# Performance work log

Hardware: AMD Instinct MI355X
Metric: run time of the kernel (lower is better)

The kernel has to match this reference:

```python
import jax, jax.numpy as jnp
import numpy as np

N_NODES = 100000
N_EDGES = 1600000
D_FEAT = 128
HIDDEN = 256
N_CLASSES = 40


def setup_inputs() -> dict:
    key = jax.random.key(0)
    ks = jax.random.split(key, 6)
    x = jax.random.normal(ks[0], (N_NODES, D_FEAT), dtype=jnp.float32)
    edge_index = jax.random.randint(ks[1], (2, N_EDGES), 0, N_NODES, dtype=jnp.int32)
    # Glorot-ish scaled weights
    w1_l = jax.random.normal(ks[2], (HIDDEN, D_FEAT), dtype=jnp.float32) / np.sqrt(D_FEAT)
    w1_r = jax.random.normal(ks[3], (HIDDEN, D_FEAT), dtype=jnp.float32) / np.sqrt(D_FEAT)
    w2_l = jax.random.normal(ks[4], (N_CLASSES, HIDDEN), dtype=jnp.float32) / np.sqrt(HIDDEN)
    w2_r = jax.random.normal(ks[5], (N_CLASSES, HIDDEN), dtype=jnp.float32) / np.sqrt(HIDDEN)
    b1_l = jnp.zeros((HIDDEN,), jnp.float32)
    b2_l = jnp.zeros((N_CLASSES,), jnp.float32)
    return {"x": x, "edge_index": edge_index, "w1_l": w1_l, "b1_l": b1_l,
            "w1_r": w1_r, "w2_l": w2_l, "b2_l": b2_l, "w2_r": w2_r}


def _sage_conv(x, src, dst, n_nodes, w_l, b_l, w_r):
    # mean aggregation of source-node features onto target nodes
    msg = x[src]                                                  # [E, d]
    agg = jax.ops.segment_sum(msg, dst, num_segments=n_nodes)     # [N, d]
    cnt = jax.ops.segment_sum(jnp.ones((dst.shape[0], 1), x.dtype), dst,
                              num_segments=n_nodes)               # [N, 1]
    agg = agg / jnp.maximum(cnt, 1.0)
    # out = lin_l(agg) + lin_r(x); lin_l has bias, lin_r does not (PyG default)
    return agg @ w_l.T + b_l + x @ w_r.T


def reference(x, edge_index, w1_l, b1_l, w1_r, w2_l, b2_l, w2_r):
    n_nodes = x.shape[0]
    src, dst = edge_index[0], edge_index[1]
    h = jax.nn.relu(_sage_conv(x, src, dst, n_nodes, w1_l, b1_l, w1_r))
    # dropout is identity in eval mode
    out = _sage_conv(h, src, dst, n_nodes, w2_l, b2_l, w2_r)
    return jax.nn.log_softmax(out, axis=1)
```

## Files before the change

kernel.cpp:

```cpp
#include <hip/hip_runtime.h>
#include <hip/hip_bf16.h>
#include <stdint.h>

#define NN 100000
#define NE 1600000
#define DF 128
#define DH 256
#define NC 40
#define BSHIFT 8
#define NBKT 391
#define EPB 8192
#define NBIN_BLOCKS ((NE + EPB - 1) / EPB)

typedef __attribute__((ext_vector_type(8))) short short8;
typedef __attribute__((ext_vector_type(4))) float f32x4;

typedef const __attribute__((address_space(1))) unsigned int* gas1;
typedef __attribute__((address_space(3))) unsigned int* las3;

__device__ __forceinline__ void gload16(const void* g, void* l) {
  __builtin_amdgcn_global_load_lds((gas1)g, (las3)l, 16, 0, 0);
}

__device__ __forceinline__ unsigned short f2bf(float f) {
  union { float f; unsigned u; } v; v.f = f;
  unsigned r = v.u + 0x7FFFu + ((v.u >> 16) & 1u);
  return (unsigned short)(r >> 16);
}
__device__ __forceinline__ float bflo(unsigned u) {
  union { unsigned u; float f; } v; v.u = u << 16; return v.f;
}
__device__ __forceinline__ float bfhi(unsigned u) {
  union { unsigned u; float f; } v; v.u = u & 0xFFFF0000u; return v.f;
}

__global__ void k_xbf16(const float* __restrict__ x, unsigned* __restrict__ xb) {
  int i = blockIdx.x * blockDim.x + threadIdx.x;
  if (i < NN * 64) {
    float2 v = ((const float2*)x)[i];
    xb[i] = ((unsigned)f2bf(v.y) << 16) | f2bf(v.x);
  }
}

__global__ __launch_bounds__(256) void k_bhist(const int* __restrict__ dst, int* __restrict__ bcnt) {
  __shared__ int h[NBKT];
  int tid = threadIdx.x;
  for (int b = tid; b < NBKT; b += 256) h[b] = 0;
  __syncthreads();
  int base = blockIdx.x * EPB;
  int n = NE - base; if (n > EPB) n = EPB;
  for (int i = tid; i < n; i += 256) atomicAdd(&h[dst[base + i] >> BSHIFT], 1);
  __syncthreads();
  for (int b = tid; b < NBKT; b += 256) if (h[b]) atomicAdd(&bcnt[b], h[b]);
}

__global__ __launch_bounds__(512) void k_bscan(const int* __restrict__ bcnt,
                                               int* __restrict__ boff, int* __restrict__ bcur) {
  __shared__ int s[512];
  int tid = threadIdx.x;
  int v = (tid < NBKT) ? bcnt[tid] : 0;
  s[tid] = v;
  __syncthreads();
  for (int off = 1; off < 512; off <<= 1) {
    int a = (tid >= off) ? s[tid - off] : 0;
    __syncthreads();
    s[tid] += a;
    __syncthreads();
  }
  int excl = s[tid] - v;
  if (tid < NBKT) { boff[tid] = excl; bcur[tid] = excl; }
  if (tid == 0) boff[NBKT] = s[511];
}

__global__ __launch_bounds__(256) void k_bin(const int* __restrict__ src, const int* __restrict__ dst,
                                             int* __restrict__ bcur, unsigned* __restrict__ pairs) {
  __shared__ int hcnt[NBKT];
  __shared__ int hbase[NBKT];
  int tid = threadIdx.x;
  for (int b = tid; b < NBKT; b += 256) hcnt[b] = 0;
  __syncthreads();
  int base = blockIdx.x * EPB;
  int n = NE - base; if (n > EPB) n = EPB;
  for (int i = tid; i < n; i += 256) atomicAdd(&hcnt[dst[base + i] >> BSHIFT], 1);
  __syncthreads();
  for (int b = tid; b < NBKT; b += 256) hbase[b] = hcnt[b] ? atomicAdd(&bcur[b], hcnt[b]) : 0;
  __syncthreads();
  for (int b = tid; b < NBKT; b += 256) hcnt[b] = 0;
  __syncthreads();
  for (int i = tid; i < n; i += 256) {
    int s = src[base + i], d = dst[base + i];
    int b = d >> BSHIFT;
    int slot = atomicAdd(&hcnt[b], 1);
    pairs[hbase[b] + slot] = (unsigned)s | ((unsigned)(d & 255) << 17);
  }
}

__global__ __launch_bounds__(256) void k_csr(const unsigned* __restrict__ pairs,
                                             const int* __restrict__ boff,
                                             int* __restrict__ row_ptr, int* __restrict__ csr) {
  __shared__ int ncnt[256];
  __shared__ int noff[256];
  int tid = threadIdx.x;
  int b = blockIdx.x;
  int base = boff[b], end = boff[b + 1];
  ncnt[tid] = 0;
  __syncthreads();
  for (int e = base + tid; e < end; e += 256) atomicAdd(&ncnt[pairs[e] >> 17], 1);
  __syncthreads();
  int v = ncnt[tid];
  noff[tid] = v;
  __syncthreads();
  for (int off = 1; off < 256; off <<= 1) {
    int a = (tid >= off) ? noff[tid - off] : 0;
    __syncthreads();
    noff[tid] += a;
    __syncthreads();
  }
  int excl = noff[tid] - v;
  __syncthreads();
  noff[tid] = excl;
  ncnt[tid] = 0;
  __syncthreads();
  int gnode = (b << BSHIFT) + tid;
  if (gnode < NN) row_ptr[gnode] = base + excl;
  if (b == NBKT - 1 && tid == 0) row_ptr[NN] = NE;
  for (int e = base + tid; e < end; e += 256) {
    unsigned p = pairs[e];
    int ld = p >> 17;
    int slot = atomicAdd(&ncnt[ld], 1);
    csr[base + noff[ld] + slot] = (int)(p & 0x1FFFFu);
  }
}

__global__ void k_packw(const float* __restrict__ w1l, const float* __restrict__ w1r,
                        const float* __restrict__ w2l, const float* __restrict__ w2r,
                        unsigned short* __restrict__ Wc, unsigned short* __restrict__ W2c) {
  int i = blockIdx.x * blockDim.x + threadIdx.x;
  if (i < 256 * 256) {
    int o = i >> 8, k = i & 255;
    float v = (k < 128) ? w1l[o * 128 + k] : w1r[o * 128 + (k - 128)];
    Wc[i] = f2bf(v);
  }
  int j = i - 256 * 256;
  if (j >= 0 && j < 80 * 256) {
    int o = j >> 8, k = j & 255;
    float v = (o < 40) ? w2l[o * 256 + k] : w2r[(o - 40) * 256 + k];
    W2c[j] = f2bf(v);
  }
}

__global__ void k_agg1(const unsigned* __restrict__ xb, const int* __restrict__ row_ptr,
                       const int* __restrict__ csr_src, unsigned* __restrict__ A1) {
  int w = threadIdx.x >> 6, lane = threadIdx.x & 63;
  int node = blockIdx.x * 4 + w;
  if (node >= NN) return;
  int rs = row_ptr[node], re = row_ptr[node + 1];
  float a0 = 0.f, a1 = 0.f;
  for (int e = rs; e < re; e += 8) {
    unsigned v[8];
#pragma unroll
    for (int j = 0; j < 8; ++j) {
      int ej = e + j;
      int idx = csr_src[ej < re ? ej : re - 1];
      unsigned t = xb[(size_t)idx * 64 + lane];
      v[j] = (ej < re) ? t : 0u;
    }
#pragma unroll
    for (int j = 0; j < 8; ++j) { a0 += bflo(v[j]); a1 += bfhi(v[j]); }
  }
  int deg = re - rs;
  float inv = 1.f / (float)(deg > 0 ? deg : 1);
  unsigned pack = ((unsigned)f2bf(a1 * inv) << 16) | f2bf(a0 * inv);
  A1[(size_t)node * 64 + lane] = pack;
}

__global__ __launch_bounds__(256) void k_fused(const unsigned short* __restrict__ A1,
                                               const unsigned short* __restrict__ XB,
                                               const unsigned short* __restrict__ Wc,
                                               const float* __restrict__ b1,
                                               const unsigned short* __restrict__ W2c,
                                               unsigned short* __restrict__ Pb,
                                               float* __restrict__ R) {
  __shared__ __align__(16) unsigned short sA[64 * 64];
  __shared__ __align__(16) unsigned short sB[256 * 64];
  __shared__ __align__(16) unsigned short sH[64 * 256];
  int tid = threadIdx.x;
  int w = tid >> 6, lane = tid & 63;
  int brow = blockIdx.x * 64;
  int wr = (w >> 1) * 32, wc = (w & 1) * 128;
  f32x4 acc[2][8] = {};

  for (int kt = 0; kt < 4; ++kt) {
    const unsigned short* srcA = (kt < 2) ? A1 : XB;
    int kcol = (kt & 1) * 64;
#pragma unroll
    for (int t = 0; t < 2; ++t) {
      int c = t * 256 + tid;
      int r = c >> 3, cc = c & 7;
      int scc = cc ^ (r & 7);
      int gr = brow + r; if (gr > NN - 1) gr = NN - 1;
      gload16(srcA + (size_t)gr * 128 + kcol + scc * 8, sA + c * 8);
    }
#pragma unroll
    for (int t = 0; t < 8; ++t) {
      int c = t * 256 + tid;
      int r = c >> 3, cc = c & 7;
      int scc = cc ^ (r & 7);
      gload16(Wc + (size_t)r * 256 + kt * 64 + scc * 8, sB + c * 8);
    }
    __syncthreads();
#pragma unroll
    for (int kg = 0; kg < 2; ++kg) {
      short8 af[2], bfr[8];
#pragma unroll
      for (int m = 0; m < 2; ++m) {
        int row = wr + m * 16 + (lane & 15);
        int cch = (kg * 4 + (lane >> 4)) ^ (row & 7);
        af[m] = *(const short8*)(sA + row * 64 + cch * 8);
      }
#pragma unroll
      for (int n = 0; n < 8; ++n) {
        int row = wc + n * 16 + (lane & 15);
        int cch = (kg * 4 + (lane >> 4)) ^ (row & 7);
        bfr[n] = *(const short8*)(sB + row * 64 + cch * 8);
      }
#pragma unroll
      for (int m = 0; m < 2; ++m)
#pragma unroll
        for (int n = 0; n < 8; ++n)
          acc[m][n] = __builtin_amdgcn_mfma_f32_16x16x32_bf16(af[m], bfr[n], acc[m][n], 0, 0, 0);
    }
    __syncthreads();
  }

  {
    int colbase = wc + (lane & 15);
    int rowb = wr + (lane >> 4) * 4;
#pragma unroll
    for (int n = 0; n < 8; ++n) {
      int col = colbase + n * 16;
      float bias = b1[col];
      int g = col >> 3, off = col & 7;
#pragma unroll
      for (int m = 0; m < 2; ++m) {
        int row0 = rowb + m * 16;
#pragma unroll
        for (int q = 0; q < 4; ++q) {
          int row = row0 + q;
          float v = acc[m][n][q] + bias;
          v = v > 0.f ? v : 0.f;
          sH[row * 256 + ((g ^ (row & 7)) << 3) + off] = f2bf(v);
        }
      }
    }
  }
  __syncthreads();

  f32x4 a2[5] = {};
  int nrow = w * 16 + (lane & 15);
  for (int kt = 0; kt < 4; ++kt) {
#pragma unroll
    for (int t = 0; t < 3; ++t) {
      int c = t * 256 + tid;
      if (c < 640) {
        int r = c >> 3, cc = c & 7;
        int scc = cc ^ (r & 7);
        gload16(W2c + (size_t)r * 256 + kt * 64 + scc * 8, sB + c * 8);
      }
    }
    __syncthreads();
#pragma unroll
    for (int kg = 0; kg < 2; ++kg) {
      int gH = kt * 8 + kg * 4 + (lane >> 4);
      short8 bf1 = *(const short8*)(sH + nrow * 256 + ((gH ^ (nrow & 7)) << 3));
      short8 af[5];
#pragma unroll
      for (int m = 0; m < 5; ++m) {
        int arow = m * 16 + (lane & 15);
        int cch = (kg * 4 + (lane >> 4)) ^ (arow & 7);
        af[m] = *(const short8*)(sB + arow * 64 + cch * 8);
      }
#pragma unroll
      for (int m = 0; m < 5; ++m)
        a2[m] = __builtin_amdgcn_mfma_f32_16x16x32_bf16(af[m], bf1, a2[m], 0, 0, 0);
    }
    __syncthreads();
  }

  int node = brow + nrow;
  if (node < NN) {
#pragma unroll
    for (int m = 0; m < 5; ++m) {
      int c0 = m * 16 + (lane >> 4) * 4;
      f32x4 v = a2[m];
      if (c0 < NC) {
        uint2 pk;
        pk.x = ((unsigned)f2bf(v[1]) << 16) | f2bf(v[0]);
        pk.y = ((unsigned)f2bf(v[3]) << 16) | f2bf(v[2]);
        *(uint2*)(Pb + (size_t)node * 64 + c0) = pk;
      } else {
        if (c0 < 64) *(uint2*)(Pb + (size_t)node * 64 + c0) = make_uint2(0u, 0u);
        *(float4*)(R + (size_t)node * NC + (c0 - NC)) = make_float4(v[0], v[1], v[2], v[3]);
      }
    }
  }
}

__global__ __launch_bounds__(256) void k_final(const unsigned short* __restrict__ Pb,
                                               const float* __restrict__ R,
                                               const int* __restrict__ row_ptr,
                                               const int* __restrict__ csr_src,
                                               const float* __restrict__ b2,
                                               float* __restrict__ out) {
  int w = threadIdx.x >> 6, lane = threadIdx.x & 63;
  int g = lane >> 4, r = lane & 15;
  int node = blockIdx.x * 4 + w;
  if (node >= NN) return;
  int rs = row_ptr[node], re = row_ptr[node + 1];
  float s0 = 0.f, s1 = 0.f, s2 = 0.f, s3 = 0.f;
  int nfull = (re - rs) >> 3;
  int e = rs + g;
  for (int it = 0; it < nfull; ++it, e += 8) {
    int sa = csr_src[e];
    int sb = csr_src[e + 4];
    uint2 va = *(const uint2*)(Pb + (size_t)sa * 64 + r * 4);
    uint2 vb = *(const uint2*)(Pb + (size_t)sb * 64 + r * 4);
    s0 += bflo(va.x) + bflo(vb.x);
    s1 += bfhi(va.x) + bfhi(vb.x);
    s2 += bflo(va.y) + bflo(vb.y);
    s3 += bfhi(va.y) + bfhi(vb.y);
  }
  if (e < re) {
    int sa = csr_src[e];
    uint2 va = *(const uint2*)(Pb + (size_t)sa * 64 + r * 4);
    s0 += bflo(va.x); s1 += bfhi(va.x); s2 += bflo(va.y); s3 += bfhi(va.y);
  }
  e += 4;
  if (e < re) {
    int sa = csr_src[e];
    uint2 va = *(const uint2*)(Pb + (size_t)sa * 64 + r * 4);
    s0 += bflo(va.x); s1 += bfhi(va.x); s2 += bflo(va.y); s3 += bfhi(va.y);
  }
  s0 += __shfl_xor(s0, 16); s0 += __shfl_xor(s0, 32);
  s1 += __shfl_xor(s1, 16); s1 += __shfl_xor(s1, 32);
  s2 += __shfl_xor(s2, 16); s2 += __shfl_xor(s2, 32);
  s3 += __shfl_xor(s3, 16); s3 += __shfl_xor(s3, 32);

  int deg = re - rs;
  float inv = 1.f / (float)(deg > 0 ? deg : 1);
  bool act = r < 10;
  float4 rr = act ? *(const float4*)(R + (size_t)node * NC + r * 4) : make_float4(0, 0, 0, 0);
  float4 bb = act ? *(const float4*)(b2 + r * 4) : make_float4(0, 0, 0, 0);
  float v0 = s0 * inv + rr.x + bb.x;
  float v1 = s1 * inv + rr.y + bb.y;
  float v2 = s2 * inv + rr.z + bb.z;
  float v3 = s3 * inv + rr.w + bb.w;
  float mx = act ? fmaxf(fmaxf(v0, v1), fmaxf(v2, v3)) : -1e30f;
#pragma unroll
  for (int o = 1; o < 16; o <<= 1) mx = fmaxf(mx, __shfl_xor(mx, o));
  float ex = act ? (__expf(v0 - mx) + __expf(v1 - mx) + __expf(v2 - mx) + __expf(v3 - mx)) : 0.f;
#pragma unroll
  for (int o = 1; o < 16; o <<= 1) ex += __shfl_xor(ex, o);
  float ls = mx + __logf(ex);
  if (g == 0 && act) {
    float4 o4 = make_float4(v0 - ls, v1 - ls, v2 - ls, v3 - ls);
    *(float4*)(out + (size_t)node * NC + r * 4) = o4;
  }
}

extern "C" void kernel_launch(void* const* d_in, const int* in_sizes, int n_in,
                              void* d_out, int out_size, void* d_ws, size_t ws_size,
                              hipStream_t stream) {
  const float* x   = (const float*)d_in[0];
  const int*   ei  = (const int*)d_in[1];
  const float* w1l = (const float*)d_in[2];
  const float* b1  = (const float*)d_in[3];
  const float* w1r = (const float*)d_in[4];
  const float* w2l = (const float*)d_in[5];
  const float* b2  = (const float*)d_in[6];
  const float* w2r = (const float*)d_in[7];
  float* out = (float*)d_out;
  const int* src = ei;
  const int* dst = ei + NE;

  char* ws = (char*)d_ws;
  size_t off = 0;
  auto alloc = [&](size_t bytes) -> char* {
    char* p = ws + off;
    off = (off + bytes + 255) & ~(size_t)255;
    return p;
  };
  int* bcnt     = (int*)alloc((size_t)(NBKT + 1) * 4);
  int* boff     = (int*)alloc((size_t)(NBKT + 1) * 4);
  int* bcur     = (int*)alloc((size_t)NBKT * 4);
  int* row_ptr  = (int*)alloc((size_t)(NN + 1) * 4);
  unsigned* pairs = (unsigned*)alloc((size_t)NE * 4);
  int* csr      = (int*)alloc((size_t)NE * 4);
  unsigned short* Wc  = (unsigned short*)alloc(256 * 256 * 2);
  unsigned short* W2c = (unsigned short*)alloc(80 * 256 * 2);
  unsigned*       xb  = (unsigned*)alloc((size_t)NN * 64 * 4);
  unsigned*       A1  = (unsigned*)alloc((size_t)NN * 64 * 4);
  unsigned short* Pb  = (unsigned short*)alloc((size_t)NN * 64 * 2);
  float*          R   = (float*)alloc((size_t)NN * NC * 4);

  hipMemsetAsync(bcnt, 0, (size_t)(NBKT + 1) * 4, stream);
  k_bhist<<<NBIN_BLOCKS, 256, 0, stream>>>(dst, bcnt);
  k_xbf16<<<(NN * 64 + 255) / 256, 256, 0, stream>>>(x, xb);
  k_bscan<<<1, 512, 0, stream>>>(bcnt, boff, bcur);
  k_bin<<<NBIN_BLOCKS, 256, 0, stream>>>(src, dst, bcur, pairs);
  k_csr<<<NBKT, 256, 0, stream>>>(pairs, boff, row_ptr, csr);
  k_packw<<<336, 256, 0, stream>>>(w1l, w1r, w2l, w2r, Wc, W2c);
  k_agg1<<<(NN + 3) / 4, 256, 0, stream>>>(xb, row_ptr, csr, A1);
  k_fused<<<(NN + 63) / 64, 256, 0, stream>>>((const unsigned short*)A1,
                                              (const unsigned short*)xb, Wc, b1, W2c, Pb, R);
  k_final<<<(NN + 3) / 4, 256, 0, stream>>>(Pb, R, row_ptr, csr, b2, out);
}
```

Before: 323.4 us.

## Pad CSR rows to multiples of eight with dummy zero node

Rebuilds the CSR so each node's neighbor list is padded to a multiple of 8 entries, filled with an index to an extra all-zero row appended to the bf16 feature and Pb buffers. Degrees are stored separately. The aggregation kernels can then drop their tail handling and bounds checks. k_agg1 now has each half-wave read a different edge with 8-byte loads and combines the halves with a shuffle. The cost is extra padded gathers (up to 7 per node), which always hit the same cached zero row, plus a larger CSR buffer with fixed per-bucket slack that assumes no bucket needs more than 2048 padding slots.

```diff
diff --git a/kernel.cpp b/kernel.cpp
--- a/kernel.cpp
+++ b/kernel.cpp
@@ -11,6 +11,7 @@
 #define NBKT 391
 #define EPB 8192
 #define NBIN_BLOCKS ((NE + EPB - 1) / EPB)
+#define BKT_SLACK 2048
 
 typedef __attribute__((ext_vector_type(8))) short short8;
 typedef __attribute__((ext_vector_type(4))) float f32x4;
@@ -36,9 +37,13 @@
 
 __global__ void k_xbf16(const float* __restrict__ x, unsigned* __restrict__ xb) {
   int i = blockIdx.x * blockDim.x + threadIdx.x;
-  if (i < NN * 64) {
-    float2 v = ((const float2*)x)[i];
-    xb[i] = ((unsigned)f2bf(v.y) << 16) | f2bf(v.x);
+  if (i < (NN + 1) * 64) {
+    unsigned pk = 0u;
+    if (i < NN * 64) {
+      float2 v = ((const float2*)x)[i];
+      pk = ((unsigned)f2bf(v.y) << 16) | f2bf(v.x);
+    }
+    xb[i] = pk;
   }
 }
 
@@ -55,7 +60,8 @@
 }
 
 __global__ __launch_bounds__(512) void k_bscan(const int* __restrict__ bcnt,
-                                               int* __restrict__ boff, int* __restrict__ bcur) {
+                                               int* __restrict__ boff, int* __restrict__ bcur,
+                                               unsigned short* __restrict__ Pb) {
   __shared__ int s[512];
   int tid = threadIdx.x;
   int v = (tid < NBKT) ? bcnt[tid] : 0;
@@ -69,7 +75,8 @@
   }
   int excl = s[tid] - v;
   if (tid < NBKT) { boff[tid] = excl; bcur[tid] = excl; }
-  if (tid == 0) boff[NBKT] = s[511];
+  if (tid == NBKT) boff[NBKT] = excl;
+  if (tid >= 448 && tid < 480) ((unsigned*)(Pb + (size_t)NN * 64))[tid - 448] = 0u;
 }
 
 __global__ __launch_bounds__(256) void k_bin(const int* __restrict__ src, const int* __restrict__ dst,
@@ -97,18 +104,21 @@
 
 __global__ __launch_bounds__(256) void k_csr(const unsigned* __restrict__ pairs,
                                              const int* __restrict__ boff,
-                                             int* __restrict__ row_ptr, int* __restrict__ csr) {
+                                             int* __restrict__ deg, int* __restrict__ row_ptr8,
+                                             int* __restrict__ csr8) {
   __shared__ int ncnt[256];
   __shared__ int noff[256];
   int tid = threadIdx.x;
   int b = blockIdx.x;
   int base = boff[b], end = boff[b + 1];
+  int base8 = base + BKT_SLACK * b;
   ncnt[tid] = 0;
   __syncthreads();
   for (int e = base + tid; e < end; e += 256) atomicAdd(&ncnt[pairs[e] >> 17], 1);
   __syncthreads();
-  int v = ncnt[tid];
-  noff[tid] = v;
+  int cnt = ncnt[tid];
+  int pcnt = (cnt + 7) & ~7;
+  noff[tid] = pcnt;
   __syncthreads();
   for (int off = 1; off < 256; off <<= 1) {
     int a = (tid >= off) ? noff[tid - off] : 0;
@@ -116,20 +126,20 @@
     noff[tid] += a;
     __syncthreads();
   }
-  int excl = noff[tid] - v;
-  __syncthreads();
-  noff[tid] = excl;
+  int pexcl = noff[tid] - pcnt;
+  __syncthreads();
+  noff[tid] = pexcl;
   ncnt[tid] = 0;
   __syncthreads();
   int gnode = (b << BSHIFT) + tid;
-  if (gnode < NN) row_ptr[gnode] = base + excl;
-  if (b == NBKT - 1 && tid == 0) row_ptr[NN] = NE;
+  if (gnode < NN) { deg[gnode] = cnt; row_ptr8[gnode] = base8 + pexcl; }
   for (int e = base + tid; e < end; e += 256) {
     unsigned p = pairs[e];
     int ld = p >> 17;
     int slot = atomicAdd(&ncnt[ld], 1);
-    csr[base + noff[ld] + slot] = (int)(p & 0x1FFFFu);
-  }
+    csr8[base8 + noff[ld] + slot] = (int)(p & 0x1FFFFu);
+  }
+  for (int k = cnt; k < pcnt; ++k) csr8[base8 + pexcl + k] = NN;
 }
 
 __global__ void k_packw(const float* __restrict__ w1l, const float* __restrict__ w1r,
@@ -149,29 +159,38 @@
   }
 }
 
-__global__ void k_agg1(const unsigned* __restrict__ xb, const int* __restrict__ row_ptr,
-                       const int* __restrict__ csr_src, unsigned* __restrict__ A1) {
+__global__ void k_agg1(const unsigned* __restrict__ xb, const int* __restrict__ row_ptr8,
+                       const int* __restrict__ deg, const int* __restrict__ csr8,
+                       unsigned* __restrict__ A1) {
   int w = threadIdx.x >> 6, lane = threadIdx.x & 63;
   int node = blockIdx.x * 4 + w;
   if (node >= NN) return;
-  int rs = row_ptr[node], re = row_ptr[node + 1];
-  float a0 = 0.f, a1 = 0.f;
-  for (int e = rs; e < re; e += 8) {
-    unsigned v[8];
-#pragma unroll
-    for (int j = 0; j < 8; ++j) {
-      int ej = e + j;
-      int idx = csr_src[ej < re ? ej : re - 1];
-      unsigned t = xb[(size_t)idx * 64 + lane];
-      v[j] = (ej < re) ? t : 0u;
-    }
-#pragma unroll
-    for (int j = 0; j < 8; ++j) { a0 += bflo(v[j]); a1 += bfhi(v[j]); }
-  }
-  int deg = re - rs;
-  float inv = 1.f / (float)(deg > 0 ? deg : 1);
-  unsigned pack = ((unsigned)f2bf(a1 * inv) << 16) | f2bf(a0 * inv);
-  A1[(size_t)node * 64 + lane] = pack;
+  int dg = deg[node];
+  int rs = row_ptr8[node];
+  int pdeg = (dg + 7) & ~7;
+  int half = lane >> 5, li = lane & 31;
+  float a0 = 0.f, a1 = 0.f, a2 = 0.f, a3 = 0.f;
+  const unsigned* xp = xb + li * 2;
+  for (int e = rs; e < rs + pdeg; e += 8) {
+#pragma unroll
+    for (int j = 0; j < 4; ++j) {
+      int idx = csr8[e + 2 * j + half];
+      uint2 v = *(const uint2*)(xp + (size_t)idx * 64);
+      a0 += bflo(v.x); a1 += bfhi(v.x);
+      a2 += bflo(v.y); a3 += bfhi(v.y);
+    }
+  }
+  a0 += __shfl_xor(a0, 32);
+  a1 += __shfl_xor(a1, 32);
+  a2 += __shfl_xor(a2, 32);
+  a3 += __shfl_xor(a3, 32);
+  if (half == 0) {
+    float inv = 1.f / (float)(dg > 0 ? dg : 1);
+    uint2 pk;
+    pk.x = ((unsigned)f2bf(a1 * inv) << 16) | f2bf(a0 * inv);
+    pk.y = ((unsigned)f2bf(a3 * inv) << 16) | f2bf(a2 * inv);
+    *(uint2*)(A1 + (size_t)node * 64 + li * 2) = pk;
+  }
 }
 
 __global__ __launch_bounds__(256) void k_fused(const unsigned short* __restrict__ A1,
@@ -308,21 +327,23 @@
 
 __global__ __launch_bounds__(256) void k_final(const unsigned short* __restrict__ Pb,
                                                const float* __restrict__ R,
-                                               const int* __restrict__ row_ptr,
-                                               const int* __restrict__ csr_src,
+                                               const int* __restrict__ row_ptr8,
+                                               const int* __restrict__ deg,
+                                               const int* __restrict__ csr8,
                                                const float* __restrict__ b2,
                                                float* __restrict__ out) {
   int w = threadIdx.x >> 6, lane = threadIdx.x & 63;
   int g = lane >> 4, r = lane & 15;
   int node = blockIdx.x * 4 + w;
   if (node >= NN) return;
-  int rs = row_ptr[node], re = row_ptr[node + 1];
+  int dg = deg[node];
+  int rs = row_ptr8[node];
+  int nfull = ((dg + 7) & ~7) >> 3;
   float s0 = 0.f, s1 = 0.f, s2 = 0.f, s3 = 0.f;
-  int nfull = (re - rs) >> 3;
   int e = rs + g;
   for (int it = 0; it < nfull; ++it, e += 8) {
-    int sa = csr_src[e];
-    int sb = csr_src[e + 4];
+    int sa = csr8[e];
+    int sb = csr8[e + 4];
     uint2 va = *(const uint2*)(Pb + (size_t)sa * 64 + r * 4);
     uint2 vb = *(const uint2*)(Pb + (size_t)sb * 64 + r * 4);
     s0 += bflo(va.x) + bflo(vb.x);
@@ -330,24 +351,12 @@
     s2 += bflo(va.y) + bflo(vb.y);
     s3 += bfhi(va.y) + bfhi(vb.y);
   }
-  if (e < re) {
-    int sa = csr_src[e];
-    uint2 va = *(const uint2*)(Pb + (size_t)sa * 64 + r * 4);
-    s0 += bflo(va.x); s1 += bfhi(va.x); s2 += bflo(va.y); s3 += bfhi(va.y);
-  }
-  e += 4;
-  if (e < re) {
-    int sa = csr_src[e];
-    uint2 va = *(const uint2*)(Pb + (size_t)sa * 64 + r * 4);
-    s0 += bflo(va.x); s1 += bfhi(va.x); s2 += bflo(va.y); s3 += bfhi(va.y);
-  }
   s0 += __shfl_xor(s0, 16); s0 += __shfl_xor(s0, 32);
   s1 += __shfl_xor(s1, 16); s1 += __shfl_xor(s1, 32);
   s2 += __shfl_xor(s2, 16); s2 += __shfl_xor(s2, 32);
   s3 += __shfl_xor(s3, 16); s3 += __shfl_xor(s3, 32);
 
-  int deg = re - rs;
-  float inv = 1.f / (float)(deg > 0 ? deg : 1);
+  float inv = 1.f / (float)(dg > 0 ? dg : 1);
   bool act = r < 10;
   float4 rr = act ? *(const float4*)(R + (size_t)node * NC + r * 4) : make_float4(0, 0, 0, 0);
   float4 bb = act ? *(const float4*)(b2 + r * 4) : make_float4(0, 0, 0, 0);
@@ -393,25 +402,26 @@
   int* bcnt     = (int*)alloc((size_t)(NBKT + 1) * 4);
   int* boff     = (int*)alloc((size_t)(NBKT + 1) * 4);
   int* bcur     = (int*)alloc((size_t)NBKT * 4);
-  int* row_ptr  = (int*)alloc((size_t)(NN + 1) * 4);
+  int* deg      = (int*)alloc((size_t)NN * 4);
+  int* row_ptr8 = (int*)alloc((size_t)NN * 4);
   unsigned* pairs = (unsigned*)alloc((size_t)NE * 4);
-  int* csr      = (int*)alloc((size_t)NE * 4);
+  int* csr8     = (int*)alloc((size_t)(NE + BKT_SLACK * NBKT + 64) * 4);
   unsigned short* Wc  = (unsigned short*)alloc(256 * 256 * 2);
   unsigned short* W2c = (unsigned short*)alloc(80 * 256 * 2);
-  unsigned*       xb  = (unsigned*)alloc((size_t)NN * 64 * 4);
+  unsigned*       xb  = (unsigned*)alloc((size_t)(NN + 1) * 64 * 4);
   unsigned*       A1  = (unsigned*)alloc((size_t)NN * 64 * 4);
-  unsigned short* Pb  = (unsigned short*)alloc((size_t)NN * 64 * 2);
+  unsigned short* Pb  = (unsigned short*)alloc((size_t)(NN + 1) * 64 * 2);
   float*          R   = (float*)alloc((size_t)NN * NC * 4);
 
   hipMemsetAsync(bcnt, 0, (size_t)(NBKT + 1) * 4, stream);
   k_bhist<<<NBIN_BLOCKS, 256, 0, stream>>>(dst, bcnt);
-  k_xbf16<<<(NN * 64 + 255) / 256, 256, 0, stream>>>(x, xb);
-  k_bscan<<<1, 512, 0, stream>>>(bcnt, boff, bcur);
+  k_xbf16<<<((NN + 1) * 64 + 255) / 256, 256, 0, stream>>>(x, xb);
+  k_bscan<<<1, 512, 0, stream>>>(bcnt, boff, bcur, Pb);
   k_bin<<<NBIN_BLOCKS, 256, 0, stream>>>(src, dst, bcur, pairs);
-  k_csr<<<NBKT, 256, 0, stream>>>(pairs, boff, row_ptr, csr);
+  k_csr<<<NBKT, 256, 0, stream>>>(pairs, boff, deg, row_ptr8, csr8);
   k_packw<<<336, 256, 0, stream>>>(w1l, w1r, w2l, w2r, Wc, W2c);
-  k_agg1<<<(NN + 3) / 4, 256, 0, stream>>>(xb, row_ptr, csr, A1);
+  k_agg1<<<(NN + 3) / 4, 256, 0, stream>>>(xb, row_ptr8, deg, csr8, A1);
   k_fused<<<(NN + 63) / 64, 256, 0, stream>>>((const unsigned short*)A1,
                                               (const unsigned short*)xb, Wc, b1, W2c, Pb, R);
-  k_final<<<(NN + 3) / 4, 256, 0, stream>>>(Pb, R, row_ptr, csr, b2, out);
-}
+  k_final<<<(NN + 3) / 4, 256, 0, stream>>>(Pb, R, row_ptr8, deg, csr8, b2, out);
+}
```

Measured after the change: 328.0 us. No clear change (+1.4%).
